# Kernel tuning notes

Hardware: AMD Instinct MI355X
Metric: run time of the kernel (lower is better)

## Reference

```python
import jax, jax.numpy as jnp
import numpy as np

TOP_K = 2


def setup_inputs() -> dict:
    key = jax.random.key(0)
    k1, k2, k3, k4 = jax.random.split(key, 4)
    B, S, D, F, E = 4, 512, 512, 2048, 16
    hidden_states = jax.random.normal(k1, (B, S, D), dtype=jnp.float32)
    gate_weight = jax.random.normal(k2, (E, D), dtype=jnp.float32) * 0.02
    w1 = jax.random.normal(k3, (E, F, D), dtype=jnp.float32) * 0.02
    w2 = jax.random.normal(k4, (E, D, F), dtype=jnp.float32) * 0.02
    return {"hidden_states": hidden_states, "gate_weight": gate_weight, "w1": w1, "w2": w2}


def reference(hidden_states, gate_weight, w1, w2):
    B, S, D = hidden_states.shape
    E = gate_weight.shape[0]
    x = hidden_states.reshape(-1, D)  # [T, D]

    # fused_top_k_routing: logits = x @ Wg^T, top-k, softmax over the k values
    gate_logits = x @ gate_weight.T  # [T, E]
    top_vals, top_idx = jax.lax.top_k(gate_logits, TOP_K)  # [T, k]
    routing_w = jax.nn.softmax(top_vals, axis=-1)  # [T, k]

    # _prepare_expert_inputs: token t goes to expert e iff e in its top-k
    mask = jnp.any(top_idx[:, :, None] == jnp.arange(E)[None, None, :], axis=1)  # [T, E] bool

    # Expert FFN on routed tokens, computed densely over (token, expert) pairs then masked.
    # h[t,e,f] = silu(x_t @ W1_e^T)
    h = jax.nn.silu(jnp.einsum('td,efd->tef', x, w1))  # [T, E, F]
    counts = jnp.sum(mask, axis=0)  # [E]
    h_sum = jnp.einsum('tef,te->ef', h, mask.astype(h.dtype))  # [E, F]
    h_mean = h_sum / jnp.maximum(counts, 1)[:, None].astype(h.dtype)

    # fused_expert_scatter_gather uses expert_outputs[e].mean(dim=0);
    # mean(W2 @ act) = W2 @ mean(act) since W2 is linear.
    y_mean = jnp.einsum('ef,edf->ed', h_mean, w2)  # [E, D]
    y_mean = jnp.where((counts > 0)[:, None], y_mean, 0.0)

    # per-token combine: sum_k w_k * mean_output[expert_k]
    out = jnp.einsum('tk,tkd->td', routing_w, y_mean[top_idx])  # [T, D]
    return out.reshape(B, S, D)
```

## Files before the change

kernel.cpp:

```cpp
#include <hip/hip_runtime.h>

#define NTOK   2048
#define DIM    512
#define FDIM   2048
#define NEXP   16
#define CAP    768
#define BT2    128
#define NTB    (CAP / BT2)

typedef __bf16 bf16x8 __attribute__((ext_vector_type(8)));
typedef __bf16 bf16x4 __attribute__((ext_vector_type(4)));
typedef float  floatx4 __attribute__((ext_vector_type(4)));

#define WS_COUNTS    0
#define WS_ZEROPAGE  1024
#define WS_TOPIDX    4096
#define WS_ROUTW     20480
#define WS_HMEAN     36864
#define WS_YMEAN     167936
#define WS_XG        200704
#define WS_ZERO_BYTES 167936

__global__ __launch_bounds__(256) void k1_route_gather(
    const float* __restrict__ x, const float* __restrict__ gw,
    int* __restrict__ counts, int* __restrict__ top_idx,
    float* __restrict__ routw, __bf16* __restrict__ Xg)
{
    __shared__ float xt[16 * DIM];
    __shared__ float lg[16][17];
    __shared__ int   gdst[16][2];
    const int tid = threadIdx.x;
    const int t0  = blockIdx.x * 16;

    {
        const float4* src = (const float4*)(x + (size_t)t0 * DIM);
        float4* dst = (float4*)xt;
        #pragma unroll
        for (int i = 0; i < 8; ++i) dst[i * 256 + tid] = src[i * 256 + tid];
    }
    __syncthreads();

    {
        const int tl = tid >> 4, e = tid & 15;
        const float4* xr = (const float4*)(xt + tl * DIM);
        const float4* gr = (const float4*)(gw + e * DIM);
        float acc = 0.f;
        #pragma unroll 8
        for (int j = 0; j < DIM / 4; ++j) {
            float4 a = xr[j], b = gr[j];
            acc += a.x * b.x + a.y * b.y + a.z * b.z + a.w * b.w;
        }
        lg[tl][e] = acc;
    }
    __syncthreads();

    if (tid < 16) {
        const int tl = tid;
        float v0 = -1e30f, v1 = -1e30f; int i0 = 0, i1 = 0;
        #pragma unroll
        for (int e = 0; e < NEXP; ++e) {
            float v = lg[tl][e];
            if (v > v0)      { v1 = v0; i1 = i0; v0 = v; i0 = e; }
            else if (v > v1) { v1 = v;  i1 = e; }
        }
        float e1 = __expf(v1 - v0);
        float w0 = 1.f / (1.f + e1);
        float w1 = 1.f - w0;
        const int t = t0 + tl;
        top_idx[t * 2]     = i0; top_idx[t * 2 + 1] = i1;
        routw[t * 2]       = w0; routw[t * 2 + 1]   = w1;
        int p0 = atomicAdd(counts + i0, 1);
        int p1 = atomicAdd(counts + i1, 1);
        gdst[tl][0] = (p0 < CAP) ? (i0 * CAP + p0) : -1;
        gdst[tl][1] = (p1 < CAP) ? (i1 * CAP + p1) : -1;
    }
    __syncthreads();

    #pragma unroll
    for (int it = 0; it < 16; ++it) {
        int s   = it * 256 + tid;
        int job = s >> 7, el = s & 127;
        int tl  = job >> 1, k = job & 1;
        int dst = gdst[tl][k];
        if (dst >= 0) {
            float4 v = ((const float4*)(xt + tl * DIM))[el];
            bf16x4 o = { (__bf16)v.x, (__bf16)v.y, (__bf16)v.z, (__bf16)v.w };
            *(bf16x4*)(Xg + (size_t)dst * DIM + el * 4) = o;
        }
    }
}

__global__ __launch_bounds__(256) void k2_expert_ffn(
    const float* __restrict__ w1, const __bf16* __restrict__ Xg,
    const int* __restrict__ counts, const __bf16* __restrict__ zp,
    float* __restrict__ hmean)
{
    __shared__ __align__(16) __bf16 w1s[8 * 65 * 8];
    __shared__ __align__(16) __bf16 xs[8 * 129 * 8];
    __shared__ float hred[64][2];

    const int tid = threadIdx.x;
    const int bid = blockIdx.x;
    const int tb  = bid >> 9;
    const int rem = bid & 511;
    const int e   = rem & 15;
    const int f0  = (rem >> 4) * 64;
    const int cnt = min(counts[e], CAP);
    if (tb * BT2 >= cnt) return;
    const float inv = 1.f / (float)cnt;

    const int wv   = tid >> 6;
    const int lane = tid & 63;
    const int q    = lane >> 4;
    const int l15  = lane & 15;
    const int fsub = (wv & 1) * 32;
    const int tsub = (wv >> 1) * 64;

    floatx4 acc[2][4];
    #pragma unroll
    for (int a = 0; a < 2; ++a)
        #pragma unroll
        for (int b = 0; b < 4; ++b) acc[a][b] = (floatx4)0.f;

    for (int c = 0; c < 8; ++c) {
        const int d0 = c * 64;
        __syncthreads();
        #pragma unroll
        for (int it = 0; it < 2; ++it) {
            int s = it * 256 + tid;
            int f = s >> 3, g = s & 7;
            const float* src = w1 + ((size_t)(e * FDIM + f0 + f)) * DIM + d0 + g * 8;
            float4 a = ((const float4*)src)[0];
            float4 b = ((const float4*)src)[1];
            bf16x8 v;
            v[0] = (__bf16)a.x; v[1] = (__bf16)a.y; v[2] = (__bf16)a.z; v[3] = (__bf16)a.w;
            v[4] = (__bf16)b.x; v[5] = (__bf16)b.y; v[6] = (__bf16)b.z; v[7] = (__bf16)b.w;
            *(bf16x8*)(w1s + ((size_t)g * 65 + f) * 8) = v;
        }
        {
            const int kg = tid & 7;
            const int r0 = tid >> 3;
            #pragma unroll
            for (int it = 0; it < 4; ++it) {
                int t = it * 32 + r0;
                int r = tb * BT2 + t;
                const __bf16* src = (r < cnt)
                    ? (Xg + ((size_t)(e * CAP + r)) * DIM + d0 + kg * 8)
                    : zp;
                uint4 d = *(const uint4*)src;
                *(uint4*)(xs + ((size_t)kg * 129 + t) * 8) = d;
            }
        }
        __syncthreads();
        #pragma unroll
        for (int ks = 0; ks < 2; ++ks) {
            const int kg = ks * 4 + q;
            bf16x8 af0 = *(const bf16x8*)(w1s + (kg * 65 + fsub + l15) * 8);
            bf16x8 af1 = *(const bf16x8*)(w1s + (kg * 65 + fsub + 16 + l15) * 8);
            #pragma unroll
            for (int tt = 0; tt < 4; ++tt) {
                bf16x8 bfr = *(const bf16x8*)(xs + (kg * 129 + tsub + tt * 16 + l15) * 8);
                acc[0][tt] = __builtin_amdgcn_mfma_f32_16x16x32_bf16(af0, bfr, acc[0][tt], 0, 0, 0);
                acc[1][tt] = __builtin_amdgcn_mfma_f32_16x16x32_bf16(af1, bfr, acc[1][tt], 0, 0, 0);
            }
        }
    }

    float hs[8];
    #pragma unroll
    for (int i = 0; i < 8; ++i) hs[i] = 0.f;
    #pragma unroll
    for (int fa = 0; fa < 2; ++fa)
        #pragma unroll
        for (int tt = 0; tt < 4; ++tt)
            #pragma unroll
            for (int r = 0; r < 4; ++r) {
                float v = acc[fa][tt][r];
                hs[fa * 4 + r] += v / (1.f + __expf(-v));
            }

    #pragma unroll
    for (int i = 0; i < 8; ++i) {
        float v = hs[i];
        v += __shfl_xor(v, 1);
        v += __shfl_xor(v, 2);
        v += __shfl_xor(v, 4);
        v += __shfl_xor(v, 8);
        hs[i] = v;
    }
    if (l15 == 0) {
        #pragma unroll
        for (int fa = 0; fa < 2; ++fa)
            #pragma unroll
            for (int r = 0; r < 4; ++r) {
                int row = fsub + fa * 16 + q * 4 + r;
                hred[row][wv >> 1] = hs[fa * 4 + r];
            }
    }
    __syncthreads();
    if (tid < 64)
        atomicAdd(hmean + (size_t)e * FDIM + f0 + tid,
                  (hred[tid][0] + hred[tid][1]) * inv);
}

__global__ __launch_bounds__(256) void k3_ymean(
    const float* __restrict__ w2, const float* __restrict__ hmean,
    const int* __restrict__ counts, float* __restrict__ ymean)
{
    __shared__ float hl[FDIM];
    const int tid = threadIdx.x;
    const int bid = blockIdx.x;
    const int e   = bid >> 7;
    const int d0  = (bid & 127) * 4;

    {
        const float4* hg = (const float4*)(hmean + (size_t)e * FDIM);
        float4* hl4 = (float4*)hl;
        hl4[tid]       = hg[tid];
        hl4[256 + tid] = hg[256 + tid];
    }
    __syncthreads();

    const int wv = tid >> 6, lane = tid & 63;
    const int d = d0 + wv;
    const float4* wr  = (const float4*)(w2 + ((size_t)e * DIM + d) * FDIM);
    const float4* hl4 = (const float4*)hl;
    float acc = 0.f;
    #pragma unroll
    for (int i = 0; i < 8; ++i) {
        float4 a = wr[i * 64 + lane];
        float4 h = hl4[i * 64 + lane];
        acc += a.x * h.x + a.y * h.y + a.z * h.z + a.w * h.w;
    }
    #pragma unroll
    for (int m = 1; m < 64; m <<= 1) acc += __shfl_xor(acc, m);
    if (lane == 0)
        ymean[e * DIM + d] = (counts[e] > 0) ? acc : 0.f;
}

__global__ __launch_bounds__(256) void k4_combine(
    const int* __restrict__ top_idx, const float* __restrict__ routw,
    const float* __restrict__ ymean, float* __restrict__ out)
{
    const int idx = blockIdx.x * 256 + threadIdx.x;
    const int t = idx >> 7;
    const int c = idx & 127;
    const int i0 = top_idx[t * 2], i1 = top_idx[t * 2 + 1];
    const float w0 = routw[t * 2], w1 = routw[t * 2 + 1];
    float4 a = ((const float4*)(ymean + (size_t)i0 * DIM))[c];
    float4 b = ((const float4*)(ymean + (size_t)i1 * DIM))[c];
    float4 o;
    o.x = w0 * a.x + w1 * b.x;
    o.y = w0 * a.y + w1 * b.y;
    o.z = w0 * a.z + w1 * b.z;
    o.w = w0 * a.w + w1 * b.w;
    ((float4*)out)[idx] = o;
}

extern "C" void kernel_launch(void* const* d_in, const int* in_sizes, int n_in,
                              void* d_out, int out_size, void* d_ws, size_t ws_size,
                              hipStream_t stream)
{
    (void)in_sizes; (void)n_in; (void)out_size; (void)ws_size;
    const float* x  = (const float*)d_in[0];
    const float* gw = (const float*)d_in[1];
    const float* w1 = (const float*)d_in[2];
    const float* w2 = (const float*)d_in[3];
    float* out = (float*)d_out;

    char* ws = (char*)d_ws;
    int*    counts  = (int*)   (ws + WS_COUNTS);
    const __bf16* zp = (const __bf16*)(ws + WS_ZEROPAGE);
    int*    top_idx = (int*)   (ws + WS_TOPIDX);
    float*  routw   = (float*) (ws + WS_ROUTW);
    float*  hmean   = (float*) (ws + WS_HMEAN);
    float*  ymean   = (float*) (ws + WS_YMEAN);
    __bf16* Xg      = (__bf16*)(ws + WS_XG);

    hipMemsetAsync(d_ws, 0, WS_ZERO_BYTES, stream);

    k1_route_gather<<<dim3(NTOK / 16), dim3(256), 0, stream>>>(x, gw, counts, top_idx, routw, Xg);
    k2_expert_ffn  <<<dim3(NTB * 32 * NEXP), dim3(256), 0, stream>>>(w1, Xg, counts, zp, hmean);
    k3_ymean       <<<dim3(NEXP * 128), dim3(256), 0, stream>>>(w2, hmean, counts, ymean);
    k4_combine     <<<dim3(NTOK * DIM / 4 / 256), dim3(256), 0, stream>>>(top_idx, routw, ymean, out);
}
```

Baseline: 211.1 us.

## Double-buffer expert FFN tiles with async global-to-LDS loads and k-major Xg layout

Changes the gathered token buffer Xg to a k-group-major layout ([e][d/8][CAP][8]) so each expert tile can be copied straight into LDS with global_load_lds. The expert FFN kernel double-buffers the W1 and X tiles so the next chunk is staged while MFMAs run on the current one. Partial tail tiles fall back to regular zero-filled loads, which removes the zero page. This adds LDS usage and relies on the async copy finishing by the single barrier at the end of each iteration.

Result: slower. 216.5 us (+2.6%).

```diff
diff --git a/kernel.cpp b/kernel.cpp
--- a/kernel.cpp
+++ b/kernel.cpp
@@ -9,11 +9,9 @@
 #define NTB    (CAP / BT2)
 
 typedef __bf16 bf16x8 __attribute__((ext_vector_type(8)));
-typedef __bf16 bf16x4 __attribute__((ext_vector_type(4)));
 typedef float  floatx4 __attribute__((ext_vector_type(4)));
 
 #define WS_COUNTS    0
-#define WS_ZEROPAGE  1024
 #define WS_TOPIDX    4096
 #define WS_ROUTW     20480
 #define WS_HMEAN     36864
@@ -21,6 +19,13 @@
 #define WS_XG        200704
 #define WS_ZERO_BYTES 167936
 
+
+__device__ __forceinline__ void async_lds16(const void* g, void* l) {
+    __builtin_amdgcn_global_load_lds(
+        (const __attribute__((address_space(1))) void*)g,
+        (__attribute__((address_space(3))) void*)l, 16, 0, 0);
+}
+
 __global__ __launch_bounds__(256) void k1_route_gather(
     const float* __restrict__ x, const float* __restrict__ gw,
     int* __restrict__ counts, int* __restrict__ top_idx,
@@ -28,7 +33,8 @@
 {
     __shared__ float xt[16 * DIM];
     __shared__ float lg[16][17];
-    __shared__ int   gdst[16][2];
+    __shared__ int   gde[16][2];
+    __shared__ int   gdp[16][2];
     const int tid = threadIdx.x;
     const int t0  = blockIdx.x * 16;
 
@@ -71,42 +77,48 @@
         routw[t * 2]       = w0; routw[t * 2 + 1]   = w1;
         int p0 = atomicAdd(counts + i0, 1);
         int p1 = atomicAdd(counts + i1, 1);
-        gdst[tl][0] = (p0 < CAP) ? (i0 * CAP + p0) : -1;
-        gdst[tl][1] = (p1 < CAP) ? (i1 * CAP + p1) : -1;
-    }
-    __syncthreads();
-
-    #pragma unroll
-    for (int it = 0; it < 16; ++it) {
-        int s   = it * 256 + tid;
-        int job = s >> 7, el = s & 127;
-        int tl  = job >> 1, k = job & 1;
-        int dst = gdst[tl][k];
-        if (dst >= 0) {
-            float4 v = ((const float4*)(xt + tl * DIM))[el];
-            bf16x4 o = { (__bf16)v.x, (__bf16)v.y, (__bf16)v.z, (__bf16)v.w };
-            *(bf16x4*)(Xg + (size_t)dst * DIM + el * 4) = o;
+        gde[tl][0] = (p0 < CAP) ? i0 : -1;  gdp[tl][0] = p0;
+        gde[tl][1] = (p1 < CAP) ? i1 : -1;  gdp[tl][1] = p1;
+    }
+    __syncthreads();
+
+    #pragma unroll
+    for (int it = 0; it < 8; ++it) {
+        int j   = it * 256 + tid;
+        int row = j >> 6, s = j & 63;
+        int tl  = row >> 1, k = row & 1;
+        int e   = gde[tl][k];
+        if (e >= 0) {
+            int p = gdp[tl][k];
+            const float* srcf = xt + tl * DIM + s * 8;
+            float4 a = *(const float4*)srcf;
+            float4 b = *(const float4*)(srcf + 4);
+            bf16x8 v;
+            v[0] = (__bf16)a.x; v[1] = (__bf16)a.y; v[2] = (__bf16)a.z; v[3] = (__bf16)a.w;
+            v[4] = (__bf16)b.x; v[5] = (__bf16)b.y; v[6] = (__bf16)b.z; v[7] = (__bf16)b.w;
+            *(bf16x8*)(Xg + ((size_t)(e * 64 + s) * CAP + p) * 8) = v;
         }
     }
 }
 
 __global__ __launch_bounds__(256) void k2_expert_ffn(
     const float* __restrict__ w1, const __bf16* __restrict__ Xg,
-    const int* __restrict__ counts, const __bf16* __restrict__ zp,
-    float* __restrict__ hmean)
-{
-    __shared__ __align__(16) __bf16 w1s[8 * 65 * 8];
-    __shared__ __align__(16) __bf16 xs[8 * 129 * 8];
+    const int* __restrict__ counts, float* __restrict__ hmean)
+{
+    __shared__ __align__(16) __bf16 w1s[2][8 * 65 * 8];
+    __shared__ __align__(16) __bf16 xs[2][8 * 128 * 8];
     __shared__ float hred[64][2];
 
     const int tid = threadIdx.x;
     const int bid = blockIdx.x;
     const int tb  = bid >> 9;
-    const int rem = bid & 511;
-    const int e   = rem & 15;
-    const int f0  = (rem >> 4) * 64;
+    const int rem9 = bid & 511;
+    const int e   = rem9 & 15;
+    const int f0  = (rem9 >> 4) * 64;
     const int cnt = min(counts[e], CAP);
     if (tb * BT2 >= cnt) return;
+    const bool tail = (tb * BT2 + BT2 > cnt);
+    const int rem  = cnt - tb * BT2;
     const float inv = 1.f / (float)cnt;
 
     const int wv   = tid >> 6;
@@ -115,6 +127,7 @@
     const int l15  = lane & 15;
     const int fsub = (wv & 1) * 32;
     const int tsub = (wv >> 1) * 64;
+    const int wvbase = tid & 192;
 
     floatx4 acc[2][4];
     #pragma unroll
@@ -122,48 +135,64 @@
         #pragma unroll
         for (int b = 0; b < 4; ++b) acc[a][b] = (floatx4)0.f;
 
-    for (int c = 0; c < 8; ++c) {
-        const int d0 = c * 64;
-        __syncthreads();
+    auto stage = [&](int cc, int nb) {
+        const int d0 = cc * 64;
         #pragma unroll
         for (int it = 0; it < 2; ++it) {
             int s = it * 256 + tid;
-            int f = s >> 3, g = s & 7;
-            const float* src = w1 + ((size_t)(e * FDIM + f0 + f)) * DIM + d0 + g * 8;
+            int f = s >> 3, g8 = s & 7;
+            const float* src = w1 + ((size_t)(e * FDIM + f0 + f)) * DIM + d0 + g8 * 8;
             float4 a = ((const float4*)src)[0];
             float4 b = ((const float4*)src)[1];
             bf16x8 v;
             v[0] = (__bf16)a.x; v[1] = (__bf16)a.y; v[2] = (__bf16)a.z; v[3] = (__bf16)a.w;
             v[4] = (__bf16)b.x; v[5] = (__bf16)b.y; v[6] = (__bf16)b.z; v[7] = (__bf16)b.w;
-            *(bf16x8*)(w1s + ((size_t)g * 65 + f) * 8) = v;
-        }
-        {
-            const int kg = tid & 7;
-            const int r0 = tid >> 3;
-            #pragma unroll
-            for (int it = 0; it < 4; ++it) {
-                int t = it * 32 + r0;
-                int r = tb * BT2 + t;
-                const __bf16* src = (r < cnt)
-                    ? (Xg + ((size_t)(e * CAP + r)) * DIM + d0 + kg * 8)
-                    : zp;
-                uint4 d = *(const uint4*)src;
-                *(uint4*)(xs + ((size_t)kg * 129 + t) * 8) = d;
-            }
-        }
-        __syncthreads();
+            *(bf16x8*)(&w1s[nb][((size_t)g8 * 65 + f) * 8]) = v;
+        }
+        if (!tail) {
+            #pragma unroll
+            for (int j = 0; j < 4; ++j) {
+                int s = j * 256 + tid;
+                int kg = s >> 7, tl = s & 127;
+                const __bf16* g = Xg + (((size_t)(e * 64 + cc * 8 + kg)) * CAP + tb * BT2 + tl) * 8;
+                __bf16* l = &xs[nb][(size_t)(j * 256 + wvbase) * 8];
+                async_lds16(g, l);
+            }
+        } else {
+            #pragma unroll
+            for (int j = 0; j < 4; ++j) {
+                int s = j * 256 + tid;
+                int kg = s >> 7, tl = s & 127;
+                uint4 v = make_uint4(0u, 0u, 0u, 0u);
+                if (tl < rem)
+                    v = *(const uint4*)(Xg + (((size_t)(e * 64 + cc * 8 + kg)) * CAP + tb * BT2 + tl) * 8);
+                *(uint4*)(&xs[nb][(size_t)s * 8]) = v;
+            }
+        }
+    };
+
+    stage(0, 0);
+    __syncthreads();
+
+    int cur = 0;
+    for (int c = 0; c < 8; ++c) {
+        if (c < 7) stage(c + 1, cur ^ 1);
+        const __bf16* w1c = w1s[cur];
+        const __bf16* xc  = xs[cur];
         #pragma unroll
         for (int ks = 0; ks < 2; ++ks) {
             const int kg = ks * 4 + q;
-            bf16x8 af0 = *(const bf16x8*)(w1s + (kg * 65 + fsub + l15) * 8);
-            bf16x8 af1 = *(const bf16x8*)(w1s + (kg * 65 + fsub + 16 + l15) * 8);
+            bf16x8 af0 = *(const bf16x8*)(w1c + ((size_t)kg * 65 + fsub + l15) * 8);
+            bf16x8 af1 = *(const bf16x8*)(w1c + ((size_t)kg * 65 + fsub + 16 + l15) * 8);
             #pragma unroll
             for (int tt = 0; tt < 4; ++tt) {
-                bf16x8 bfr = *(const bf16x8*)(xs + (kg * 129 + tsub + tt * 16 + l15) * 8);
+                bf16x8 bfr = *(const bf16x8*)(xc + ((size_t)kg * 128 + tsub + tt * 16 + l15) * 8);
                 acc[0][tt] = __builtin_amdgcn_mfma_f32_16x16x32_bf16(af0, bfr, acc[0][tt], 0, 0, 0);
                 acc[1][tt] = __builtin_amdgcn_mfma_f32_16x16x32_bf16(af1, bfr, acc[1][tt], 0, 0, 0);
             }
         }
+        __syncthreads();
+        cur ^= 1;
     }
 
     float hs[8];
@@ -270,7 +299,6 @@
 
     char* ws = (char*)d_ws;
     int*    counts  = (int*)   (ws + WS_COUNTS);
-    const __bf16* zp = (const __bf16*)(ws + WS_ZEROPAGE);
     int*    top_idx = (int*)   (ws + WS_TOPIDX);
     float*  routw   = (float*) (ws + WS_ROUTW);
     float*  hmean   = (float*) (ws + WS_HMEAN);
@@ -280,7 +308,7 @@
     hipMemsetAsync(d_ws, 0, WS_ZERO_BYTES, stream);
 
     k1_route_gather<<<dim3(NTOK / 16), dim3(256), 0, stream>>>(x, gw, counts, top_idx, routw, Xg);
-    k2_expert_ffn  <<<dim3(NTB * 32 * NEXP), dim3(256), 0, stream>>>(w1, Xg, counts, zp, hmean);
+    k2_expert_ffn  <<<dim3(NTB * 32 * NEXP), dim3(256), 0, stream>>>(w1, Xg, counts, hmean);
     k3_ymean       <<<dim3(NEXP * 128), dim3(256), 0, stream>>>(w2, hmean, counts, ymean);
     k4_combine     <<<dim3(NTOK * DIM / 4 / 256), dim3(256), 0, stream>>>(top_idx, routw, ymean, out);
 }
```
